# Optimization experiments

Hardware: AMD Instinct MI355X
Metric: run time of the kernel (lower is better)

Reference implementation:

```python
import jax, jax.numpy as jnp
import numpy as np

N_TRAIN, DIM, OUT_DIM, BATCH = 16384, 64, 8, 8192


def setup_inputs() -> dict:
    key = jax.random.key(0)
    k1, k2, k3 = jax.random.split(key, 3)
    batches = jax.random.uniform(k1, (BATCH, DIM), dtype=jnp.float32)
    x_training = jax.random.uniform(k2, (N_TRAIN, DIM), dtype=jnp.float32)
    y_training = jax.random.normal(k3, (N_TRAIN, OUT_DIM), dtype=jnp.float32)
    beta = jnp.ones((1, N_TRAIN), dtype=jnp.float32) / 0.1  # matches ones/0.1 init
    return {"batches": batches, "x_training": x_training,
            "y_training": y_training, "beta": beta}


def reference(batches, x_training, y_training, beta):
    # Pairwise Euclidean distances [batch, n_train] via the expanded form
    # (avoids the O(batch*n_train*dim) repeated tensor the torch code builds).
    b2 = jnp.sum(batches * batches, axis=1, keepdims=True)        # [B, 1]
    x2 = jnp.sum(x_training * x_training, axis=1)[None, :]        # [1, N]
    sq = jnp.maximum(b2 + x2 - 2.0 * (batches @ x_training.T), 0.0)
    dist = jnp.sqrt(sq)                                           # [B, N]
    radial_val = jnp.exp(-beta * dist)                            # RBF kernel [B, N]
    psum1 = jnp.sum(radial_val, axis=1, keepdims=True)            # [B, 1]
    psum2 = radial_val @ y_training                               # [B, OUT_DIM]
    return psum2 / psum1
```

## Files before the change

kernel.cpp:

```cpp
#include <hip/hip_runtime.h>
#include <math.h>
#include <stdint.h>

#define NTRAIN 16384
#define DIM 64
#define ODIM 8
#define BATCH 8192
#define LOG2E 1.4426950408889634f

typedef float f32x16 __attribute__((ext_vector_type(16)));
typedef short short8 __attribute__((ext_vector_type(8)));
typedef _Float16 f16x8 __attribute__((ext_vector_type(8)));
typedef unsigned short u16;

static __device__ __forceinline__ u16 f2bf(float f) {
  unsigned u = __builtin_bit_cast(unsigned, f);
  u += 0x7FFFu + ((u >> 16) & 1u);
  return (u16)(u >> 16);
}
static __device__ __forceinline__ u16 f2h(float f) {
  return __builtin_bit_cast(u16, (_Float16)f);
}
static __device__ __forceinline__ float h2f(u16 h) {
  return (float)__builtin_bit_cast(_Float16, h);
}

static __device__ __forceinline__ f32x16 mfma_bf(short8 a, short8 b, f32x16 c) {
  return __builtin_amdgcn_mfma_f32_32x32x16_bf16(a, b, c, 0, 0, 0);
}
static __device__ __forceinline__ f32x16 mfma_h(f16x8 a, f16x8 b, f32x16 c) {
  return __builtin_amdgcn_mfma_f32_32x32x16_f16(a, b, c, 0, 0, 0);
}
static __device__ __forceinline__ unsigned pkbf(float a, float b) {
  unsigned d;
  asm("v_cvt_pk_bf16_f32 %0, %1, %2" : "=v"(d) : "v"(a), "v"(b));
  return d;
}
static __device__ __forceinline__ float ex2n(float x) {
  float r;
  asm("v_exp_f32 %0, -%1" : "=v"(r) : "v"(x));
  return r;
}
static __device__ __forceinline__ void plswap(unsigned& a, unsigned& b) {
  asm("v_permlane32_swap_b32 %0, %1" : "+v"(a), "+v"(b));
}

__global__ __launch_bounds__(256) void k_frag(
    const float* __restrict__ xt, const float* __restrict__ yt,
    const float* __restrict__ beta,
    u16* __restrict__ xf, u16* __restrict__ yv) {
  int tid = blockIdx.x * 256 + threadIdx.x;

  if (tid < (NTRAIN / 32) * 5 * 64) {
    int fg = tid >> 6, lane = tid & 63;
    int tile = fg / 5, f = fg % 5;
    int lr = lane & 31, hi = lane >> 5;
    uint4 u = {0, 0, 0, 0};
    if (f == 4) {
      if (hi == 0) {
        int n = tile * 32 + lr;
        float g = beta[n] * LOG2E;
        float g2v = g * g;
        const float4* r4 = (const float4*)(xt + (size_t)n * DIM);
        float s0 = 0.f, s1 = 0.f, s2 = 0.f, s3 = 0.f;
#pragma unroll
        for (int q = 0; q < DIM / 4; ++q) {
          float4 v = r4[q];
          s0 = fmaf(v.x, v.x, s0); s1 = fmaf(v.y, v.y, s1);
          s2 = fmaf(v.z, v.z, s2); s3 = fmaf(v.w, v.w, s3);
        }
        float gx2v = g2v * ((s0 + s1) + (s2 + s3));
        u16 xh = f2h(gx2v);
        u16 xl = f2h(gx2v - h2f(xh));
        u16 gh = f2h(g2v);
        u16 gl = f2h(g2v - h2f(gh));
        u.x = (unsigned)xh | ((unsigned)xl << 16);
        u.y = (unsigned)gh | ((unsigned)gh << 16);
        u.z = (unsigned)gl;
      }
    } else {
      int n = tile * 32 + lr;
      float g = beta[n] * LOG2E;
      float s2g = 2.0f * g * g;
      const float* src = xt + (size_t)n * DIM + f * 16 + hi * 8;
      unsigned e[8];
#pragma unroll
      for (int j = 0; j < 8; ++j) e[j] = f2h(s2g * src[j]);
      u.x = e[0] | (e[1] << 16); u.y = e[2] | (e[3] << 16);
      u.z = e[4] | (e[5] << 16); u.w = e[6] | (e[7] << 16);
    }
    ((uint4*)xf)[(size_t)fg * 64 + lane] = u;
    return;
  }
  tid -= (NTRAIN / 32) * 5 * 64;

  if (tid < (NTRAIN / 16) * 64) {
    int frag = tid >> 6, lane = tid & 63;
    int col = lane & 31, hi = lane >> 5;
    int n = frag * 16 + hi * 8;
    unsigned e[8];
#pragma unroll
    for (int j = 0; j < 8; ++j) {
      float v = (col == 0) ? 1.0f : ((col < 9) ? yt[(size_t)(n + j) * ODIM + (col - 1)] : 0.0f);
      e[j] = f2bf(v);
    }
    uint4 u;
    u.x = e[0] | (e[1] << 16); u.y = e[2] | (e[3] << 16);
    u.z = e[4] | (e[5] << 16); u.w = e[6] | (e[7] << 16);
    ((uint4*)yv)[(size_t)frag * 64 + lane] = u;
  }
}

#define LOAD5(X_, nbv)                                                        \
  {                                                                           \
    const size_t fb_ = (size_t)((nbv) >> 5) * 5;                              \
    _Pragma("unroll")                                                         \
    for (int f = 0; f < 5; ++f) X_[f] = xf4[(fb_ + f) * 64 + lane];           \
  }

#define COMPUTE(X_, nbv)                                                      \
  {                                                                           \
    short8 V0 = __builtin_bit_cast(short8,                                    \
                                   yv4[(size_t)((nbv) >> 4) * 64 + lane]);    \
    short8 V1 = __builtin_bit_cast(                                           \
        short8, yv4[(size_t)((nbv) >> 4) * 64 + 64 + lane]);                  \
    f32x16 sA;                                                                \
    _Pragma("unroll")                                                         \
    for (int r = 0; r < 16; ++r) sA[r] = 0.f;                                 \
    __builtin_amdgcn_s_setprio(1);                                            \
    sA = mfma_h(__builtin_bit_cast(f16x8, X_[4]), AN, sA);                    \
    _Pragma("unroll")                                                         \
    for (int ks = 0; ks < 4; ++ks)                                            \
      sA = mfma_h(__builtin_bit_cast(f16x8, X_[ks]), AH[ks], sA);             \
    __builtin_amdgcn_s_setprio(0);                                            \
    unsigned U[8];                                                            \
    _Pragma("unroll")                                                         \
    for (int p = 0; p < 8; ++p) {                                             \
      float d0 = __builtin_amdgcn_sqrtf(fabsf(sA[2 * p]));                    \
      float d1 = __builtin_amdgcn_sqrtf(fabsf(sA[2 * p + 1]));                \
      U[p] = pkbf(ex2n(d0), ex2n(d1));                                        \
    }                                                                         \
    plswap(U[0], U[2]); plswap(U[1], U[3]);                                   \
    plswap(U[4], U[6]); plswap(U[5], U[7]);                                   \
    uint4 a1 = {U[0], U[1], U[2], U[3]};                                      \
    uint4 a2 = {U[4], U[5], U[6], U[7]};                                      \
    pv = mfma_bf(__builtin_bit_cast(short8, a1), V0, pv);                     \
    pv = mfma_bf(__builtin_bit_cast(short8, a2), V1, pv);                     \
  }

__global__ __launch_bounds__(256, 4) void grnn_pass1(
    const u16* __restrict__ xf, const u16* __restrict__ yv,
    const float* __restrict__ batches,
    float* __restrict__ partial, int chunk_n, int nc) {
  const int lane = threadIdx.x & 63;
  const int lr = lane & 31, hi = lane >> 5;

  int mt, c;
  if (nc == 32) {
    const int bid = blockIdx.x;
    const int xcd = bid & 7;
    const int q = bid >> 3;
    c = xcd + 8 * (q & 3);
    mt = q >> 2;
  } else {
    mt = blockIdx.x % (BATCH / 128);
    c = blockIdx.x / (BATCH / 128);
  }
  const int mrow0 = mt * 128 + (threadIdx.x >> 6) * 32;
  const int n0 = c * chunk_n;
  const int nslab = chunk_n / 32;

  f16x8 AH[4], AN;
  const int mrow = mrow0 + lr;
  float ssum = 0.f;
#pragma unroll
  for (int ks = 0; ks < 4; ++ks) {
    const float* src = batches + (size_t)mrow * DIM + ks * 16 + hi * 8;
    float4 v0 = *(const float4*)src;
    float4 v1 = *(const float4*)(src + 4);
    AH[ks][0] = (_Float16)v0.x; AH[ks][1] = (_Float16)v0.y;
    AH[ks][2] = (_Float16)v0.z; AH[ks][3] = (_Float16)v0.w;
    AH[ks][4] = (_Float16)v1.x; AH[ks][5] = (_Float16)v1.y;
    AH[ks][6] = (_Float16)v1.z; AH[ks][7] = (_Float16)v1.w;
    ssum = fmaf(v0.x, v0.x, ssum); ssum = fmaf(v0.y, v0.y, ssum);
    ssum = fmaf(v0.z, v0.z, ssum); ssum = fmaf(v0.w, v0.w, ssum);
    ssum = fmaf(v1.x, v1.x, ssum); ssum = fmaf(v1.y, v1.y, ssum);
    ssum = fmaf(v1.z, v1.z, ssum); ssum = fmaf(v1.w, v1.w, ssum);
  }
  unsigned ua = __builtin_bit_cast(unsigned, ssum), ub = ua;
  plswap(ua, ub);
  const float b2v =
      __builtin_bit_cast(float, ua) + __builtin_bit_cast(float, ub);

#pragma unroll
  for (int j = 0; j < 8; ++j) AN[j] = (_Float16)0.0f;
  if (hi == 0) {
    _Float16 bh = (_Float16)b2v;
    _Float16 bl = (_Float16)(b2v - (float)bh);
    AN[0] = (_Float16)(-1.0f);
    AN[1] = (_Float16)(-1.0f);
    AN[2] = -bh;
    AN[3] = -bl;
    AN[4] = -bh;
  }

  f32x16 pv;
#pragma unroll
  for (int r = 0; r < 16; ++r) pv[r] = 0.f;

  const uint4* xf4 = (const uint4*)xf;
  const uint4* yv4 = (const uint4*)yv;

  uint4 Xa[5], Xb[5];
  LOAD5(Xa, n0)
  for (int s = 0; s < nslab; s += 2) {
    const int nb = n0 + s * 32;
    if (s + 1 < nslab) LOAD5(Xb, nb + 32)
    COMPUTE(Xa, nb)
    if (s + 2 < nslab) LOAD5(Xa, nb + 64)
    if (s + 1 < nslab) COMPUTE(Xb, nb + 32)
  }

  float* pc = partial + (size_t)c * 9 * BATCH;
  if (lr < 9) {
#pragma unroll
    for (int r = 0; r < 16; ++r)
      pc[(size_t)lr * BATCH + (mrow0 + (r & 3) + 8 * (r >> 2) + 4 * hi)] = pv[r];
  }
}

__global__ __launch_bounds__(256) void grnn_pass2(const float* __restrict__ partial,
                                                  float* __restrict__ out, int nc) {
  int b = blockIdx.x * 256 + threadIdx.x;
  float s1 = 0.f;
  float s2[ODIM];
#pragma unroll
  for (int j = 0; j < ODIM; ++j) s2[j] = 0.f;
  for (int cc = 0; cc < nc; ++cc) {
    const float* p = partial + (size_t)cc * 9 * BATCH;
    s1 += p[b];
#pragma unroll
    for (int j = 0; j < ODIM; ++j) s2[j] += p[(size_t)(j + 1) * BATCH + b];
  }
  const float inv = 1.f / s1;
#pragma unroll
  for (int j = 0; j < ODIM; ++j) out[(size_t)b * ODIM + j] = s2[j] * inv;
}

extern "C" void kernel_launch(void* const* d_in, const int* in_sizes, int n_in,
                              void* d_out, int out_size, void* d_ws, size_t ws_size,
                              hipStream_t stream) {
  const float* batches = (const float*)d_in[0];
  const float* xt      = (const float*)d_in[1];
  const float* yt      = (const float*)d_in[2];
  const float* beta    = (const float*)d_in[3];
  float* out = (float*)d_out;

  const size_t xf_b = (size_t)(NTRAIN / 32) * 5 * 1024;
  const size_t yv_b = (size_t)(NTRAIN / 16) * 64 * 16;
  const size_t fixed = xf_b + yv_b;
  const size_t per_chunk = (size_t)9 * BATCH * 4;

  int nc = 32;
  while (nc > 1 && fixed + (size_t)nc * per_chunk > ws_size) nc >>= 1;
  const int chunk_n = NTRAIN / nc;

  char* p = (char*)d_ws;
  u16* xf = (u16*)p;      p += xf_b;
  u16* yv = (u16*)p;      p += yv_b;
  float* partial = (float*)p;

  const int frag_threads = (NTRAIN / 32) * 5 * 64 + (NTRAIN / 16) * 64;
  k_frag<<<(frag_threads + 255) / 256, 256, 0, stream>>>(xt, yt, beta, xf, yv);
  grnn_pass1<<<(BATCH / 128) * nc, 256, 0, stream>>>(
      xf, yv, batches, partial, chunk_n, nc);
  grnn_pass2<<<BATCH / 256, 256, 0, stream>>>(partial, out, nc);
}
```

Measured before the change: 70.56 us.

## Interleave two slabs' MFMA chains and prefetch next pair before exp tail

Each loop iteration now runs the distance MFMAs for two 32-column slabs interleaved, so the two independent accumulator chains hide each other's MFMA latency. It then issues the next pair of X loads before the sqrt/exp/bf16 pack and PV MFMAs. Launch bounds drop from 4 to 3 waves-per-SIMD target to make room for the extra registers. The cost is lower occupancy, and the loop now assumes nslab is even since the second slab is no longer guarded.

After: 72.90 us. 3.3% more time.

```diff
diff --git a/kernel.cpp b/kernel.cpp
--- a/kernel.cpp
+++ b/kernel.cpp
@@ -118,37 +118,24 @@
     for (int f = 0; f < 5; ++f) X_[f] = xf4[(fb_ + f) * 64 + lane];           \
   }
 
-#define COMPUTE(X_, nbv)                                                      \
+#define TAILPV(sA_, V0_, V1_)                                                 \
   {                                                                           \
-    short8 V0 = __builtin_bit_cast(short8,                                    \
-                                   yv4[(size_t)((nbv) >> 4) * 64 + lane]);    \
-    short8 V1 = __builtin_bit_cast(                                           \
-        short8, yv4[(size_t)((nbv) >> 4) * 64 + 64 + lane]);                  \
-    f32x16 sA;                                                                \
-    _Pragma("unroll")                                                         \
-    for (int r = 0; r < 16; ++r) sA[r] = 0.f;                                 \
-    __builtin_amdgcn_s_setprio(1);                                            \
-    sA = mfma_h(__builtin_bit_cast(f16x8, X_[4]), AN, sA);                    \
-    _Pragma("unroll")                                                         \
-    for (int ks = 0; ks < 4; ++ks)                                            \
-      sA = mfma_h(__builtin_bit_cast(f16x8, X_[ks]), AH[ks], sA);             \
-    __builtin_amdgcn_s_setprio(0);                                            \
     unsigned U[8];                                                            \
     _Pragma("unroll")                                                         \
     for (int p = 0; p < 8; ++p) {                                             \
-      float d0 = __builtin_amdgcn_sqrtf(fabsf(sA[2 * p]));                    \
-      float d1 = __builtin_amdgcn_sqrtf(fabsf(sA[2 * p + 1]));                \
+      float d0 = __builtin_amdgcn_sqrtf(fabsf(sA_[2 * p]));                   \
+      float d1 = __builtin_amdgcn_sqrtf(fabsf(sA_[2 * p + 1]));               \
       U[p] = pkbf(ex2n(d0), ex2n(d1));                                        \
     }                                                                         \
     plswap(U[0], U[2]); plswap(U[1], U[3]);                                   \
     plswap(U[4], U[6]); plswap(U[5], U[7]);                                   \
     uint4 a1 = {U[0], U[1], U[2], U[3]};                                      \
     uint4 a2 = {U[4], U[5], U[6], U[7]};                                      \
-    pv = mfma_bf(__builtin_bit_cast(short8, a1), V0, pv);                     \
-    pv = mfma_bf(__builtin_bit_cast(short8, a2), V1, pv);                     \
-  }
-
-__global__ __launch_bounds__(256, 4) void grnn_pass1(
+    pv = mfma_bf(__builtin_bit_cast(short8, a1), V0_, pv);                    \
+    pv = mfma_bf(__builtin_bit_cast(short8, a2), V1_, pv);                    \
+  }
+
+__global__ __launch_bounds__(256, 3) void grnn_pass1(
     const u16* __restrict__ xf, const u16* __restrict__ yv,
     const float* __restrict__ batches,
     float* __restrict__ partial, int chunk_n, int nc) {
@@ -211,14 +198,38 @@
   const uint4* xf4 = (const uint4*)xf;
   const uint4* yv4 = (const uint4*)yv;
 
-  uint4 Xa[5], Xb[5];
-  LOAD5(Xa, n0)
+  uint4 X0[5], X1[5];
+  LOAD5(X0, n0)
+  LOAD5(X1, n0 + 32)
+
   for (int s = 0; s < nslab; s += 2) {
     const int nb = n0 + s * 32;
-    if (s + 1 < nslab) LOAD5(Xb, nb + 32)
-    COMPUTE(Xa, nb)
-    if (s + 2 < nslab) LOAD5(Xa, nb + 64)
-    if (s + 1 < nslab) COMPUTE(Xb, nb + 32)
+
+    short8 V00 = __builtin_bit_cast(short8, yv4[(size_t)(nb >> 4) * 64 + lane]);
+    short8 V01 = __builtin_bit_cast(short8, yv4[(size_t)(nb >> 4) * 64 + 64 + lane]);
+    short8 V10 = __builtin_bit_cast(short8, yv4[(size_t)(nb >> 4) * 64 + 128 + lane]);
+    short8 V11 = __builtin_bit_cast(short8, yv4[(size_t)(nb >> 4) * 64 + 192 + lane]);
+
+    f32x16 sA0, sA1;
+#pragma unroll
+    for (int r = 0; r < 16; ++r) { sA0[r] = 0.f; sA1[r] = 0.f; }
+    __builtin_amdgcn_s_setprio(1);
+    sA0 = mfma_h(__builtin_bit_cast(f16x8, X0[4]), AN, sA0);
+    sA1 = mfma_h(__builtin_bit_cast(f16x8, X1[4]), AN, sA1);
+#pragma unroll
+    for (int ks = 0; ks < 4; ++ks) {
+      sA0 = mfma_h(__builtin_bit_cast(f16x8, X0[ks]), AH[ks], sA0);
+      sA1 = mfma_h(__builtin_bit_cast(f16x8, X1[ks]), AH[ks], sA1);
+    }
+    __builtin_amdgcn_s_setprio(0);
+
+    if (s + 2 < nslab) {
+      LOAD5(X0, nb + 64)
+      LOAD5(X1, nb + 96)
+    }
+
+    TAILPV(sA0, V00, V01)
+    TAILPV(sA1, V10, V11)
   }
 
   float* pc = partial + (size_t)c * 9 * BATCH;
```

## Switch distance and weighting MFMAs from 32x32x16 to 16x16x32 tiles

Applied to the files above, without the earlier changes.

Replaces the 32x32x16 MFMA scheme with 16x16x32 f16/bf16 MFMAs. Each wave now handles 16 batch rows, and two 16-row training slabs are paired so that one bf16 MFMA applies the RBF weights to y. The fragment layouts in k_frag, the grid size (twice as many blocks) and the launch bound (occupancy 6) change to match, and the permlane swaps are removed. The aim is to cut the padding waste in the K=8+ output reduction and the per-wave register footprint so more waves can hide exp/sqrt latency. The trade-off is doubled reloading of training fragments across more blocks and more loads per useful FLOP.

Result: slower. 87.65 us (+24.2%).

```diff
diff --git a/kernel.cpp b/kernel.cpp
--- a/kernel.cpp
+++ b/kernel.cpp
@@ -8,41 +8,38 @@
 #define BATCH 8192
 #define LOG2E 1.4426950408889634f
 
-typedef float f32x16 __attribute__((ext_vector_type(16)));
+typedef float f32x4 __attribute__((ext_vector_type(4)));
+typedef _Float16 f16x8 __attribute__((ext_vector_type(8)));
 typedef short short8 __attribute__((ext_vector_type(8)));
-typedef _Float16 f16x8 __attribute__((ext_vector_type(8)));
 typedef unsigned short u16;
 
+static __device__ __forceinline__ u16 f2h(float f) {
+  return __builtin_bit_cast(u16, (_Float16)f);
+}
+static __device__ __forceinline__ float h2f(u16 h) {
+  return (float)__builtin_bit_cast(_Float16, h);
+}
 static __device__ __forceinline__ u16 f2bf(float f) {
   unsigned u = __builtin_bit_cast(unsigned, f);
   u += 0x7FFFu + ((u >> 16) & 1u);
   return (u16)(u >> 16);
 }
-static __device__ __forceinline__ u16 f2h(float f) {
-  return __builtin_bit_cast(u16, (_Float16)f);
-}
-static __device__ __forceinline__ float h2f(u16 h) {
-  return (float)__builtin_bit_cast(_Float16, h);
-}
-
-static __device__ __forceinline__ f32x16 mfma_bf(short8 a, short8 b, f32x16 c) {
-  return __builtin_amdgcn_mfma_f32_32x32x16_bf16(a, b, c, 0, 0, 0);
-}
-static __device__ __forceinline__ f32x16 mfma_h(f16x8 a, f16x8 b, f32x16 c) {
-  return __builtin_amdgcn_mfma_f32_32x32x16_f16(a, b, c, 0, 0, 0);
+
+static __device__ __forceinline__ f32x4 mfma_h32(f16x8 a, f16x8 b, f32x4 c) {
+  return __builtin_amdgcn_mfma_f32_16x16x32_f16(a, b, c, 0, 0, 0);
+}
+static __device__ __forceinline__ f32x4 mfma_bf32(short8 a, short8 b, f32x4 c) {
+  return __builtin_amdgcn_mfma_f32_16x16x32_bf16(a, b, c, 0, 0, 0);
+}
+static __device__ __forceinline__ float ex2n(float x) {
+  float r;
+  asm("v_exp_f32 %0, -%1" : "=v"(r) : "v"(x));
+  return r;
 }
 static __device__ __forceinline__ unsigned pkbf(float a, float b) {
   unsigned d;
   asm("v_cvt_pk_bf16_f32 %0, %1, %2" : "=v"(d) : "v"(a), "v"(b));
   return d;
-}
-static __device__ __forceinline__ float ex2n(float x) {
-  float r;
-  asm("v_exp_f32 %0, -%1" : "=v"(r) : "v"(x));
-  return r;
-}
-static __device__ __forceinline__ void plswap(unsigned& a, unsigned& b) {
-  asm("v_permlane32_swap_b32 %0, %1" : "+v"(a), "+v"(b));
 }
 
 __global__ __launch_bounds__(256) void k_frag(
@@ -51,14 +48,14 @@
     u16* __restrict__ xf, u16* __restrict__ yv) {
   int tid = blockIdx.x * 256 + threadIdx.x;
 
-  if (tid < (NTRAIN / 32) * 5 * 64) {
+  if (tid < (NTRAIN / 16) * 3 * 64) {
     int fg = tid >> 6, lane = tid & 63;
-    int tile = fg / 5, f = fg % 5;
-    int lr = lane & 31, hi = lane >> 5;
+    int tile = fg / 3, f = fg % 3;
+    int lr = lane & 15, lg = lane >> 4;
+    int n = tile * 16 + lr;
     uint4 u = {0, 0, 0, 0};
-    if (f == 4) {
-      if (hi == 0) {
-        int n = tile * 32 + lr;
+    if (f == 2) {
+      if (lg == 0) {
         float g = beta[n] * LOG2E;
         float g2v = g * g;
         const float4* r4 = (const float4*)(xt + (size_t)n * DIM);
@@ -79,10 +76,9 @@
         u.z = (unsigned)gl;
       }
     } else {
-      int n = tile * 32 + lr;
       float g = beta[n] * LOG2E;
       float s2g = 2.0f * g * g;
-      const float* src = xt + (size_t)n * DIM + f * 16 + hi * 8;
+      const float* src = xt + (size_t)n * DIM + f * 32 + lg * 8;
       unsigned e[8];
 #pragma unroll
       for (int j = 0; j < 8; ++j) e[j] = f2h(s2g * src[j]);
@@ -92,68 +88,56 @@
     ((uint4*)xf)[(size_t)fg * 64 + lane] = u;
     return;
   }
-  tid -= (NTRAIN / 32) * 5 * 64;
-
-  if (tid < (NTRAIN / 16) * 64) {
-    int frag = tid >> 6, lane = tid & 63;
-    int col = lane & 31, hi = lane >> 5;
-    int n = frag * 16 + hi * 8;
+  tid -= (NTRAIN / 16) * 3 * 64;
+
+  if (tid < (NTRAIN / 32) * 64) {
+    int t = tid >> 6, lane = tid & 63;
+    int col = lane & 15, lg = lane >> 4;
     unsigned e[8];
 #pragma unroll
     for (int j = 0; j < 8; ++j) {
-      float v = (col == 0) ? 1.0f : ((col < 9) ? yt[(size_t)(n + j) * ODIM + (col - 1)] : 0.0f);
+      int n = t * 32 + ((j < 4) ? (lg * 4 + j) : (16 + lg * 4 + (j - 4)));
+      float v = (col == 0) ? 1.0f
+                           : ((col < 9) ? yt[(size_t)n * ODIM + (col - 1)] : 0.0f);
       e[j] = f2bf(v);
     }
     uint4 u;
     u.x = e[0] | (e[1] << 16); u.y = e[2] | (e[3] << 16);
     u.z = e[4] | (e[5] << 16); u.w = e[6] | (e[7] << 16);
-    ((uint4*)yv)[(size_t)frag * 64 + lane] = u;
-  }
-}
-
-#define LOAD5(X_, nbv)                                                        \
+    ((uint4*)yv)[(size_t)t * 64 + lane] = u;
+  }
+}
+
+#define LOADX3(X_, nbv)                                                       \
   {                                                                           \
-    const size_t fb_ = (size_t)((nbv) >> 5) * 5;                              \
-    _Pragma("unroll")                                                         \
-    for (int f = 0; f < 5; ++f) X_[f] = xf4[(fb_ + f) * 64 + lane];           \
-  }
-
-#define COMPUTE(X_, nbv)                                                      \
+    const size_t fb_ = (size_t)((nbv) >> 4) * 3;                              \
+    X_[0] = xf4[(fb_ + 0) * 64 + lane];                                       \
+    X_[1] = xf4[(fb_ + 1) * 64 + lane];                                       \
+    X_[2] = xf4[(fb_ + 2) * 64 + lane];                                       \
+  }
+
+#define SCOMP(X_, U0_, U1_)                                                   \
   {                                                                           \
-    short8 V0 = __builtin_bit_cast(short8,                                    \
-                                   yv4[(size_t)((nbv) >> 4) * 64 + lane]);    \
-    short8 V1 = __builtin_bit_cast(                                           \
-        short8, yv4[(size_t)((nbv) >> 4) * 64 + 64 + lane]);                  \
-    f32x16 sA;                                                                \
-    _Pragma("unroll")                                                         \
-    for (int r = 0; r < 16; ++r) sA[r] = 0.f;                                 \
+    f32x4 sA = {0.f, 0.f, 0.f, 0.f};                                          \
     __builtin_amdgcn_s_setprio(1);                                            \
-    sA = mfma_h(__builtin_bit_cast(f16x8, X_[4]), AN, sA);                    \
-    _Pragma("unroll")                                                         \
-    for (int ks = 0; ks < 4; ++ks)                                            \
-      sA = mfma_h(__builtin_bit_cast(f16x8, X_[ks]), AH[ks], sA);             \
+    sA = mfma_h32(__builtin_bit_cast(f16x8, X_[2]), BN, sA);                  \
+    sA = mfma_h32(__builtin_bit_cast(f16x8, X_[0]), BH[0], sA);               \
+    sA = mfma_h32(__builtin_bit_cast(f16x8, X_[1]), BH[1], sA);               \
     __builtin_amdgcn_s_setprio(0);                                            \
-    unsigned U[8];                                                            \
-    _Pragma("unroll")                                                         \
-    for (int p = 0; p < 8; ++p) {                                             \
-      float d0 = __builtin_amdgcn_sqrtf(fabsf(sA[2 * p]));                    \
-      float d1 = __builtin_amdgcn_sqrtf(fabsf(sA[2 * p + 1]));                \
-      U[p] = pkbf(ex2n(d0), ex2n(d1));                                        \
-    }                                                                         \
-    plswap(U[0], U[2]); plswap(U[1], U[3]);                                   \
-    plswap(U[4], U[6]); plswap(U[5], U[7]);                                   \
-    uint4 a1 = {U[0], U[1], U[2], U[3]};                                      \
-    uint4 a2 = {U[4], U[5], U[6], U[7]};                                      \
-    pv = mfma_bf(__builtin_bit_cast(short8, a1), V0, pv);                     \
-    pv = mfma_bf(__builtin_bit_cast(short8, a2), V1, pv);                     \
-  }
-
-__global__ __launch_bounds__(256, 4) void grnn_pass1(
+    float w0 = ex2n(__builtin_amdgcn_sqrtf(fabsf(sA[0])));                    \
+    float w1 = ex2n(__builtin_amdgcn_sqrtf(fabsf(sA[1])));                    \
+    float w2 = ex2n(__builtin_amdgcn_sqrtf(fabsf(sA[2])));                    \
+    float w3 = ex2n(__builtin_amdgcn_sqrtf(fabsf(sA[3])));                    \
+    U0_ = pkbf(w0, w1);                                                       \
+    U1_ = pkbf(w2, w3);                                                       \
+  }
+
+__global__ __launch_bounds__(256, 6) void grnn_pass1(
     const u16* __restrict__ xf, const u16* __restrict__ yv,
     const float* __restrict__ batches,
     float* __restrict__ partial, int chunk_n, int nc) {
   const int lane = threadIdx.x & 63;
-  const int lr = lane & 31, hi = lane >> 5;
+  const int lr = lane & 15, lg = lane >> 4;
 
   int mt, c;
   if (nc == 32) {
@@ -163,69 +147,77 @@
     c = xcd + 8 * (q & 3);
     mt = q >> 2;
   } else {
-    mt = blockIdx.x % (BATCH / 128);
-    c = blockIdx.x / (BATCH / 128);
-  }
-  const int mrow0 = mt * 128 + (threadIdx.x >> 6) * 32;
+    mt = blockIdx.x % (BATCH / 64);
+    c = blockIdx.x / (BATCH / 64);
+  }
+  const int mbase = mt * 64 + (threadIdx.x >> 6) * 16;
   const int n0 = c * chunk_n;
-  const int nslab = chunk_n / 32;
-
-  f16x8 AH[4], AN;
-  const int mrow = mrow0 + lr;
+  const int npair = chunk_n / 32;
+
+  f16x8 BH[2], BN;
+  const int mrow = mbase + lr;
   float ssum = 0.f;
 #pragma unroll
-  for (int ks = 0; ks < 4; ++ks) {
-    const float* src = batches + (size_t)mrow * DIM + ks * 16 + hi * 8;
+  for (int ks = 0; ks < 2; ++ks) {
+    const float* src = batches + (size_t)mrow * DIM + ks * 32 + lg * 8;
     float4 v0 = *(const float4*)src;
     float4 v1 = *(const float4*)(src + 4);
-    AH[ks][0] = (_Float16)v0.x; AH[ks][1] = (_Float16)v0.y;
-    AH[ks][2] = (_Float16)v0.z; AH[ks][3] = (_Float16)v0.w;
-    AH[ks][4] = (_Float16)v1.x; AH[ks][5] = (_Float16)v1.y;
-    AH[ks][6] = (_Float16)v1.z; AH[ks][7] = (_Float16)v1.w;
+    BH[ks][0] = (_Float16)v0.x; BH[ks][1] = (_Float16)v0.y;
+    BH[ks][2] = (_Float16)v0.z; BH[ks][3] = (_Float16)v0.w;
+    BH[ks][4] = (_Float16)v1.x; BH[ks][5] = (_Float16)v1.y;
+    BH[ks][6] = (_Float16)v1.z; BH[ks][7] = (_Float16)v1.w;
     ssum = fmaf(v0.x, v0.x, ssum); ssum = fmaf(v0.y, v0.y, ssum);
     ssum = fmaf(v0.z, v0.z, ssum); ssum = fmaf(v0.w, v0.w, ssum);
     ssum = fmaf(v1.x, v1.x, ssum); ssum = fmaf(v1.y, v1.y, ssum);
     ssum = fmaf(v1.z, v1.z, ssum); ssum = fmaf(v1.w, v1.w, ssum);
   }
-  unsigned ua = __builtin_bit_cast(unsigned, ssum), ub = ua;
-  plswap(ua, ub);
-  const float b2v =
-      __builtin_bit_cast(float, ua) + __builtin_bit_cast(float, ub);
-
-#pragma unroll
-  for (int j = 0; j < 8; ++j) AN[j] = (_Float16)0.0f;
-  if (hi == 0) {
+  ssum += __shfl_xor(ssum, 16);
+  ssum += __shfl_xor(ssum, 32);
+  const float b2v = ssum;
+
+#pragma unroll
+  for (int j = 0; j < 8; ++j) BN[j] = (_Float16)0.0f;
+  if (lg == 0) {
     _Float16 bh = (_Float16)b2v;
     _Float16 bl = (_Float16)(b2v - (float)bh);
-    AN[0] = (_Float16)(-1.0f);
-    AN[1] = (_Float16)(-1.0f);
-    AN[2] = -bh;
-    AN[3] = -bl;
-    AN[4] = -bh;
-  }
-
-  f32x16 pv;
-#pragma unroll
-  for (int r = 0; r < 16; ++r) pv[r] = 0.f;
+    BN[0] = (_Float16)(-1.0f);
+    BN[1] = (_Float16)(-1.0f);
+    BN[2] = -bh;
+    BN[3] = -bl;
+    BN[4] = -bh;
+  }
+
+  f32x4 pv = {0.f, 0.f, 0.f, 0.f};
 
   const uint4* xf4 = (const uint4*)xf;
   const uint4* yv4 = (const uint4*)yv;
 
-  uint4 Xa[5], Xb[5];
-  LOAD5(Xa, n0)
-  for (int s = 0; s < nslab; s += 2) {
-    const int nb = n0 + s * 32;
-    if (s + 1 < nslab) LOAD5(Xb, nb + 32)
-    COMPUTE(Xa, nb)
-    if (s + 2 < nslab) LOAD5(Xa, nb + 64)
-    if (s + 1 < nslab) COMPUTE(Xb, nb + 32)
+  uint4 Xa[3], Xb[3], Vp, Vn;
+  LOADX3(Xa, n0)
+  LOADX3(Xb, n0 + 16)
+  Vp = yv4[(size_t)(n0 >> 5) * 64 + lane];
+
+  for (int p = 0; p < npair; ++p) {
+    const int nb = n0 + p * 32;
+    unsigned UA0, UA1, UB0, UB1;
+    SCOMP(Xa, UA0, UA1)
+    if (p + 1 < npair) LOADX3(Xa, nb + 32)
+    SCOMP(Xb, UB0, UB1)
+    if (p + 1 < npair) {
+      LOADX3(Xb, nb + 48)
+      Vn = yv4[(size_t)((nb + 32) >> 5) * 64 + lane];
+    }
+    uint4 pa = {UA0, UA1, UB0, UB1};
+    pv = mfma_bf32(__builtin_bit_cast(short8, pa),
+                   __builtin_bit_cast(short8, Vp), pv);
+    Vp = Vn;
   }
 
   float* pc = partial + (size_t)c * 9 * BATCH;
   if (lr < 9) {
 #pragma unroll
-    for (int r = 0; r < 16; ++r)
-      pc[(size_t)lr * BATCH + (mrow0 + (r & 3) + 8 * (r >> 2) + 4 * hi)] = pv[r];
+    for (int r = 0; r < 4; ++r)
+      pc[(size_t)lr * BATCH + (mbase + lg * 4 + r)] = pv[r];
   }
 }
 
@@ -256,8 +248,8 @@
   const float* beta    = (const float*)d_in[3];
   float* out = (float*)d_out;
 
-  const size_t xf_b = (size_t)(NTRAIN / 32) * 5 * 1024;
-  const size_t yv_b = (size_t)(NTRAIN / 16) * 64 * 16;
+  const size_t xf_b = (size_t)(NTRAIN / 16) * 3 * 1024;
+  const size_t yv_b = (size_t)(NTRAIN / 32) * 64 * 16;
   const size_t fixed = xf_b + yv_b;
   const size_t per_chunk = (size_t)9 * BATCH * 4;
 
@@ -270,9 +262,9 @@
   u16* yv = (u16*)p;      p += yv_b;
   float* partial = (float*)p;
 
-  const int frag_threads = (NTRAIN / 32) * 5 * 64 + (NTRAIN / 16) * 64;
+  const int frag_threads = (NTRAIN / 16) * 3 * 64 + (NTRAIN / 32) * 64;
   k_frag<<<(frag_threads + 255) / 256, 256, 0, stream>>>(xt, yt, beta, xf, yv);
-  grnn_pass1<<<(BATCH / 128) * nc, 256, 0, stream>>>(
+  grnn_pass1<<<(BATCH / 64) * nc, 256, 0, stream>>>(
       xf, yv, batches, partial, chunk_n, nc);
   grnn_pass2<<<BATCH / 256, 256, 0, stream>>>(partial, out, nc);
 }
```
